# Performance work log

Measured on AMD Instinct MI355X. Metric: run time of the kernel, lower is better.

## Reference

```python
import jax, jax.numpy as jnp
import numpy as np

NUM_HEADS = 8
KEY_DIM = 32
ATTN_RATIO = 4
RESOLUTION = 7
VAL_DIM = KEY_DIM * ATTN_RATIO  # 128
SCALE = KEY_DIM ** (-0.5)


def _bias_idxs():
    # (2, N) grid positions, N = resolution^2
    r = RESOLUTION
    gh, gw = np.meshgrid(np.arange(r), np.arange(r), indexing='ij')
    pos = np.stack([gh, gw], 0).reshape(2, -1)
    rel = np.abs(pos[:, :, None] - pos[:, None, :])
    return jnp.asarray(rel[0] * r + rel[1], dtype=jnp.int32)  # (N, N)


def setup_inputs() -> dict:
    key = jax.random.key(0)
    ks = jax.random.split(key, 4)
    B, N, D = 2048, RESOLUTION * RESOLUTION, 384
    qkv_out = KEY_DIM * NUM_HEADS * 2 + VAL_DIM * NUM_HEADS  # 1536
    return {
        'x': jax.random.normal(ks[0], (B, N, D), jnp.float32),
        'qkv_kernel': jax.random.normal(ks[1], (D, qkv_out), jnp.float32) * 0.02,
        'qkv_bias': jnp.zeros((qkv_out,), jnp.float32),
        'proj_kernel': jax.random.normal(ks[2], (VAL_DIM * NUM_HEADS, D), jnp.float32) * 0.02,
        'proj_bias': jnp.zeros((D,), jnp.float32),
        'attention_biases': jax.random.normal(ks[3], (NUM_HEADS, N), jnp.float32) * 0.02,
    }


def reference(x, qkv_kernel, qkv_bias, proj_kernel, proj_bias, attention_biases):
    B, N, _ = x.shape
    idxs = _bias_idxs()  # (N, N) int32
    qkv = jnp.matmul(x, qkv_kernel) + qkv_bias            # (B, N, 1536)
    qkv = qkv.reshape(B, N, NUM_HEADS, -1).transpose(0, 2, 1, 3)  # (B, H, N, 2k+v)
    q = qkv[..., :KEY_DIM]
    k = qkv[..., KEY_DIM:2 * KEY_DIM]
    v = qkv[..., 2 * KEY_DIM:]
    attn = jnp.einsum('bhnd,bhmd->bhnm', q, k) * SCALE    # (B, H, N, N)
    bias = attention_biases[:, idxs]                       # (H, N, N) gather
    attn = jax.nn.softmax(attn + bias, axis=-1)
    out = jnp.einsum('bhnm,bhmd->bhnd', attn, v)           # (B, H, N, val_dim)
    out = out.transpose(0, 2, 1, 3).reshape(B, N, NUM_HEADS * VAL_DIM)
    return jnp.matmul(out, proj_kernel) + proj_bias
```

## Files before the change

kernel.cpp:

```cpp
#include <hip/hip_runtime.h>
#include <hip/hip_bf16.h>

using bf16x8 = short __attribute__((ext_vector_type(8)));
using f32x16 = float __attribute__((ext_vector_type(16)));

#define MROWS 100352
#define SCALE_Q 0.17677669529663687f
#define XCAST_BLOCKS 18816

static __device__ __forceinline__ unsigned short f2bs(float f){
  unsigned u = __builtin_bit_cast(unsigned, f);
  unsigned r = (u + 0x7FFFu + ((u >> 16) & 1u)) >> 16;
  return (unsigned short)r;
}
static __device__ __forceinline__ unsigned packbf(float a, float b){
  return (unsigned)f2bs(a) | ((unsigned)f2bs(b) << 16);
}

__global__ void k_prep(const float* __restrict__ x, const float* __restrict__ qkvW,
                       const float* __restrict__ qkvB, const float* __restrict__ projW,
                       const float* __restrict__ ab,
                       short* __restrict__ xb, short* __restrict__ WqkvT, short* __restrict__ WpT,
                       float* __restrict__ bqkv, float* __restrict__ bias_expT){
  const int bi = blockIdx.x;
  if (bi < XCAST_BLOCKS){
    const int i = bi*256 + threadIdx.x;
    const float4 u0 = *reinterpret_cast<const float4*>(x + (size_t)i*8);
    const float4 u1 = *reinterpret_cast<const float4*>(x + (size_t)i*8 + 4);
    bf16x8 t;
    t[0]=(short)f2bs(u0.x); t[1]=(short)f2bs(u0.y); t[2]=(short)f2bs(u0.z); t[3]=(short)f2bs(u0.w);
    t[4]=(short)f2bs(u1.x); t[5]=(short)f2bs(u1.y); t[6]=(short)f2bs(u1.z); t[7]=(short)f2bs(u1.w);
    *reinterpret_cast<bf16x8*>(xb + (size_t)i*8) = t;
    return;
  }
  int i = (bi - XCAST_BLOCKS)*256 + threadIdx.x;
  if (i < 1536*384){
    int c = i/384, f = i - c*384;
    int src; float sc = 1.0f;
    if (c < 512){ src = (c>>6)*192 + (c&63); if ((c&63) < 32) sc = SCALE_Q; }
    else        { int dv = c - 512; src = (dv>>7)*192 + 64 + (dv&127); }
    WqkvT[i] = (short)f2bs(qkvW[f*1536 + src] * sc);
    return;
  }
  i -= 1536*384;
  if (i < 384*1024){
    int j = i/1024, m = i - j*1024;
    WpT[i] = (short)f2bs(projW[m*384 + j]);
    return;
  }
  i -= 384*1024;
  if (i < 1536){
    int c = i; int src; float sc = 1.0f;
    if (c < 512){ src = (c>>6)*192 + (c&63); if ((c&63) < 32) sc = SCALE_Q; }
    else        { int dv = c - 512; src = (dv>>7)*192 + 64 + (dv&127); }
    bqkv[c] = qkvB[src] * sc;
    return;
  }
  i -= 1536;
  if (i < 8*49*64){
    int h = i / (49*64), rem = i - h*(49*64);
    int n = rem >> 6, r = rem & 63;
    float v = 0.0f;
    if (r < 49){
      int rh = r/7, rw = r - rh*7, ch = n/7, cw = n - ch*7;
      int dh = rh>ch?rh-ch:ch-rh, dw = rw>cw?rw-cw:cw-rw;
      v = ab[h*49 + dh*7 + dw];
    }
    bias_expT[i] = v;
  }
}

template<int KTOT, int NT, int NSLAB, bool F32OUT>
__global__ __launch_bounds__(512) void k_gemm(const short* __restrict__ A,
                                              const short* __restrict__ Bw,
                                              const float* __restrict__ bias,
                                              void* __restrict__ Cout, int ldc){
  constexpr int BN = NT*128;
  __shared__ short Alds[128*64];
  __shared__ short Blds[BN*64];
  const int lane = threadIdx.x & 63, w = threadIdx.x >> 6;
  const int hi = lane >> 5, l31 = lane & 31;
  const int wm = w >> 2, wn = w & 3;

  const int nwg = NSLAB * 784;
  const int lin = blockIdx.x + NSLAB * blockIdx.y;
  const int swz = (lin & 7) * (nwg >> 3) + (lin >> 3);
  const int slab = swz % NSLAB, panel = swz / NSLAB;
  const size_t R0 = (size_t)panel * 128, C0 = (size_t)slab * BN;

  f32x16 acc[2][NT];
  #pragma unroll
  for (int mt=0; mt<2; ++mt)
    #pragma unroll
    for (int nt=0; nt<NT; ++nt) acc[mt][nt] = (f32x16)0.0f;

  const int srow = lane >> 3;
  const int sG   = ((lane & 7) ^ srow) * 8;
  const short* aG = A  + (R0 + (size_t)(w*8 + srow))*KTOT + sG;
  const short* bG = Bw + (C0 + (size_t)(w*8 + srow))*KTOT + sG;

  constexpr int NK = KTOT/64;
  for (int kt=0; kt<NK; ++kt){
    #pragma unroll
    for (int j=0; j<2; ++j)
      __builtin_amdgcn_global_load_lds(
        (const unsigned int __attribute__((address_space(1)))*)(aG + (size_t)j*64*KTOT + kt*64),
        (unsigned int __attribute__((address_space(3)))*)(&Alds[(j*64 + w*8)*64]), 16, 0, 0);
    #pragma unroll
    for (int j=0; j<2*NT; ++j)
      __builtin_amdgcn_global_load_lds(
        (const unsigned int __attribute__((address_space(1)))*)(bG + (size_t)j*64*KTOT + kt*64),
        (unsigned int __attribute__((address_space(3)))*)(&Blds[(j*64 + w*8)*64]), 16, 0, 0);
    __syncthreads();
    #pragma unroll
    for (int ks=0; ks<4; ++ks){
      bf16x8 aF[2], bF[NT];
      #pragma unroll
      for (int mt=0; mt<2; ++mt){
        const int rA = wm*64 + mt*32 + l31;
        aF[mt] = *reinterpret_cast<const bf16x8*>(
                   (const char*)Alds + rA*128 + ((((ks<<1)|hi) ^ (rA&7))<<4));
      }
      #pragma unroll
      for (int nt=0; nt<NT; ++nt){
        const int rB = wn*(NT*32) + nt*32 + l31;
        bF[nt] = *reinterpret_cast<const bf16x8*>(
                   (const char*)Blds + rB*128 + ((((ks<<1)|hi) ^ (rB&7))<<4));
      }
      #pragma unroll
      for (int mt=0; mt<2; ++mt)
        #pragma unroll
        for (int nt=0; nt<NT; ++nt)
          acc[mt][nt] = __builtin_amdgcn_mfma_f32_32x32x16_bf16(aF[mt], bF[nt], acc[mt][nt], 0,0,0);
    }
    __syncthreads();
  }

  #pragma unroll
  for (int nt=0; nt<NT; ++nt){
    const int c = (int)C0 + wn*(NT*32) + nt*32 + l31;
    const float bb = bias[c];
    #pragma unroll
    for (int mt=0; mt<2; ++mt){
      const size_t rbase = R0 + wm*64 + mt*32;
      #pragma unroll
      for (int rg=0; rg<16; ++rg){
        const size_t r = rbase + (rg&3) + 8*(rg>>2) + 4*hi;
        if constexpr (F32OUT) ((float*)Cout)[r*ldc + c] = acc[mt][nt][rg] + bb;
        else                  ((short*)Cout)[r*ldc + c] = (short)f2bs(acc[mt][nt][rg] + bb);
      }
    }
  }
}

__global__ __launch_bounds__(256) void k_proj4(const short* __restrict__ A,
                                               const short* __restrict__ Bw,
                                               const float* __restrict__ bias,
                                               float* __restrict__ out){
  __shared__ short Alds[128*64];
  __shared__ short Blds[128*64];
  const int lane = threadIdx.x & 63, w = threadIdx.x >> 6;
  const int hi = lane >> 5, l31 = lane & 31;
  const int wm = w >> 1, wn = w & 1;

  const int nwg = 3 * 784;
  const int lin = blockIdx.x + 3 * blockIdx.y;
  const int swz = (lin & 7) * (nwg >> 3) + (lin >> 3);
  const int slab = swz % 3, panel = swz / 3;
  const size_t R0 = (size_t)panel * 128, C0 = (size_t)slab * 128;

  f32x16 acc[2][2];
  acc[0][0]=(f32x16)0.f; acc[0][1]=(f32x16)0.f; acc[1][0]=(f32x16)0.f; acc[1][1]=(f32x16)0.f;

  const int srow = lane >> 3;
  const int sG   = ((lane & 7) ^ srow) * 8;
  const short* aG = A  + (R0 + (size_t)(w*8 + srow))*1024 + sG;
  const short* bG = Bw + (C0 + (size_t)(w*8 + srow))*1024 + sG;

  for (int kt=0; kt<16; ++kt){
    #pragma unroll
    for (int j=0; j<4; ++j){
      __builtin_amdgcn_global_load_lds(
        (const unsigned int __attribute__((address_space(1)))*)(aG + (size_t)j*32*1024 + kt*64),
        (unsigned int __attribute__((address_space(3)))*)(&Alds[(j*32 + w*8)*64]), 16, 0, 0);
      __builtin_amdgcn_global_load_lds(
        (const unsigned int __attribute__((address_space(1)))*)(bG + (size_t)j*32*1024 + kt*64),
        (unsigned int __attribute__((address_space(3)))*)(&Blds[(j*32 + w*8)*64]), 16, 0, 0);
    }
    __syncthreads();
    #pragma unroll
    for (int ks=0; ks<4; ++ks){
      bf16x8 aF[2], bF[2];
      #pragma unroll
      for (int mt=0; mt<2; ++mt){
        const int rA = wm*64 + mt*32 + l31;
        aF[mt] = *reinterpret_cast<const bf16x8*>(
                   (const char*)Alds + rA*128 + ((((ks<<1)|hi) ^ (rA&7))<<4));
      }
      #pragma unroll
      for (int nt=0; nt<2; ++nt){
        const int rB = wn*64 + nt*32 + l31;
        bF[nt] = *reinterpret_cast<const bf16x8*>(
                   (const char*)Blds + rB*128 + ((((ks<<1)|hi) ^ (rB&7))<<4));
      }
      #pragma unroll
      for (int mt=0; mt<2; ++mt)
        #pragma unroll
        for (int nt=0; nt<2; ++nt)
          acc[mt][nt] = __builtin_amdgcn_mfma_f32_32x32x16_bf16(aF[mt], bF[nt], acc[mt][nt], 0,0,0);
    }
    __syncthreads();
  }

  #pragma unroll
  for (int nt=0; nt<2; ++nt){
    const int c = (int)C0 + wn*64 + nt*32 + l31;
    const float bb = bias[c];
    #pragma unroll
    for (int mt=0; mt<2; ++mt){
      const size_t rbase = R0 + wm*64 + mt*32;
      #pragma unroll
      for (int rg=0; rg<16; ++rg){
        const size_t r = rbase + (rg&3) + 8*(rg>>2) + 4*hi;
        out[r*384 + c] = acc[mt][nt][rg] + bb;
      }
    }
  }
}

__global__ __launch_bounds__(256) void k_attn(const short* __restrict__ qkvbuf,
                                              const float* __restrict__ bias_expT, short* __restrict__ aout){
  const int lane = threadIdx.x & 63, w = threadIdx.x >> 6;
  const int hi = lane >> 5, l31 = lane & 31;
  const int b = blockIdx.x, hg = blockIdx.y;
  const int h = hg*4 + w;

  __shared__ short vlds[4*49*136];

  for (int i=0; i<13; ++i){
    const int n = i*4 + w;
    if (n < 49){
      const bf16x8 vv = *reinterpret_cast<const bf16x8*>(qkvbuf + (b*49+n)*1536 + 512 + hg*512 + lane*8);
      const int hh = lane >> 4;
      const int d0 = ((lane & 15) * 8) ^ (((n>>3)&1) << 5);
      *reinterpret_cast<bf16x8*>(&vlds[(hh*49 + n)*136 + d0]) = vv;
    }
  }
  __syncthreads();

  bf16x8 kf[2][2];
  #pragma unroll
  for (int mt=0; mt<2; ++mt){
    const int n = 32*mt + l31;
    #pragma unroll
    for (int ks=0; ks<2; ++ks)
      kf[mt][ks] = (n < 49)
        ? *reinterpret_cast<const bf16x8*>(qkvbuf + (b*49+n)*1536 + h*64 + 32 + ks*16 + hi*8)
        : (bf16x8)(short)0;
  }
  const short* vb = &vlds[w*49*136];
  const int dxbase = hi << 5;

  for (int rb=0; rb<2; ++rb){
    const int r = 32*rb + l31;
    bf16x8 qf[2];
    #pragma unroll
    for (int ks=0; ks<2; ++ks)
      qf[ks] = (r < 49)
        ? *reinterpret_cast<const bf16x8*>(qkvbuf + (b*49+r)*1536 + h*64 + ks*16 + hi*8)
        : (bf16x8)(short)0;

    f32x16 s[2];
    s[0] = (f32x16)0.0f; s[1] = (f32x16)0.0f;
    #pragma unroll
    for (int ks=0; ks<2; ++ks){
      s[0] = __builtin_amdgcn_mfma_f32_32x32x16_bf16(kf[0][ks], qf[ks], s[0], 0, 0, 0);
      s[1] = __builtin_amdgcn_mfma_f32_32x32x16_bf16(kf[1][ks], qf[ks], s[1], 0, 0, 0);
    }

    float mloc = -3.0e38f;
    #pragma unroll
    for (int mt=0; mt<2; ++mt)
      #pragma unroll
      for (int rg=0; rg<16; ++rg){
        const int n = 32*mt + (rg&3) + 8*(rg>>2) + 4*hi;
        float v = s[mt][rg];
        v = (n < 49) ? v + bias_expT[(h*49 + n)*64 + r] : -1.0e30f;
        s[mt][rg] = v;
        mloc = fmaxf(mloc, v);
      }
    const float mrow = fmaxf(mloc, __shfl_xor(mloc, 32));
    float sloc = 0.0f;
    #pragma unroll
    for (int mt=0; mt<2; ++mt)
      #pragma unroll
      for (int rg=0; rg<16; ++rg){
        const float p = __expf(s[mt][rg] - mrow);
        s[mt][rg] = p; sloc += p;
      }
    const float inv = 1.0f / (sloc + __shfl_xor(sloc, 32));
    #pragma unroll
    for (int mt=0; mt<2; ++mt)
      #pragma unroll
      for (int rg=0; rg<16; ++rg) s[mt][rg] *= inv;

    unsigned pk[8][2];
    #pragma unroll
    for (int o=0; o<8; ++o){
      const int mt = o>>2, base = 4*(o&3);
      pk[o][0] = packbf(s[mt][base+0], s[mt][base+1]);
      pk[o][1] = packbf(s[mt][base+2], s[mt][base+3]);
    }
    bf16x8 af[4];
    #pragma unroll
    for (int ks=0; ks<4; ++ks){
      const unsigned e0 = pk[2*ks][0],   e1 = pk[2*ks][1];
      const unsigned o0 = pk[2*ks+1][0], o1 = pk[2*ks+1][1];
      const unsigned own0 = hi ? o0 : e0, own1 = hi ? o1 : e1;
      const unsigned oth0 = hi ? e0 : o0, oth1 = hi ? e1 : o1;
      const unsigned sw0 = __shfl_xor(oth0, 32), sw1 = __shfl_xor(oth1, 32);
      const unsigned lo0 = hi ? sw0 : own0, lo1 = hi ? sw1 : own1;
      const unsigned h0  = hi ? own0 : sw0, h1  = hi ? own1 : sw1;
      union { bf16x8 v; unsigned u[4]; } t;
      t.u[0]=lo0; t.u[1]=lo1; t.u[2]=h0; t.u[3]=h1;
      af[ks] = t.v;
    }

    #pragma unroll
    for (int dt=0; dt<4; ++dt){
      const int dx = (dt*32 + l31) ^ dxbase;
      f32x16 acc = (f32x16)0.0f;
      #pragma unroll
      for (int ks=0; ks<4; ++ks){
        bf16x8 t;
        if (ks < 3){
          const int nb = ks*16 + hi*8;
          #pragma unroll
          for (int j=0; j<8; ++j) t[j] = vb[(nb + j)*136 + dx];
        } else {
          #pragma unroll
          for (int j=0; j<8; ++j) t[j] = 0;
          if (hi == 0) t[0] = vb[48*136 + (dt*32 + l31)];
        }
        acc = __builtin_amdgcn_mfma_f32_32x32x16_bf16(af[ks], t, acc, 0, 0, 0);
      }
      #pragma unroll
      for (int rg=0; rg<16; ++rg){
        const int rr = 32*rb + (rg&3) + 8*(rg>>2) + 4*hi;
        if (rr < 49)
          aout[(b*49+rr)*1024 + h*128 + dt*32 + l31] = (short)f2bs(acc[rg]);
      }
    }
  }
}

extern "C" void kernel_launch(void* const* d_in, const int* in_sizes, int n_in,
                              void* d_out, int out_size, void* d_ws, size_t ws_size,
                              hipStream_t stream) {
  const float* x     = (const float*)d_in[0];
  const float* qkvW  = (const float*)d_in[1];
  const float* qkvB  = (const float*)d_in[2];
  const float* projW = (const float*)d_in[3];
  const float* projB = (const float*)d_in[4];
  const float* ab    = (const float*)d_in[5];

  char* ws = (char*)d_ws;
  short* aoutb = (short*)ws;
  short* xb    = (short*)ws;
  size_t off = (size_t)MROWS*1024*2;
  short* qkvbuf = (short*)(ws + off); off += (size_t)MROWS*1536*2;
  short* WqkvT  = (short*)(ws + off); off += (size_t)1536*384*2;
  short* WpT    = (short*)(ws + off); off += (size_t)384*1024*2;
  float* bqkv   = (float*)(ws + off); off += (size_t)1536*4;
  float* bias_expT = (float*)(ws + off); off += (size_t)8*49*64*4;
  if (ws_size < off) return;

  const int conv_total = 1536*384 + 384*1024 + 1536 + 8*49*64;
  const int prep_blocks = XCAST_BLOCKS + (conv_total + 255)/256;
  k_prep<<<prep_blocks, 256, 0, stream>>>(x, qkvW, qkvB, projW, ab,
                                          xb, WqkvT, WpT, bqkv, bias_expT);
  k_gemm<384, 2, 6, false><<<dim3(6, 784), 512, 0, stream>>>(xb, WqkvT, bqkv, qkvbuf, 1536);
  k_attn<<<dim3(2048, 2), 256, 0, stream>>>(qkvbuf, bias_expT, aoutb);
  k_proj4<<<dim3(3, 784), 256, 0, stream>>>(aoutb, WpT, projB, (float*)d_out);
}
```

Baseline: 505.0 us.

## Rewrite QKV GEMM with 256x256 tiles and triple-buffered LDS pipeline

Replaces the generic QKV GEMM with a dedicated kernel that uses 256x256 output tiles, K-steps of 32, and three LDS buffers. Global-to-LDS loads for step kt+2 are issued between the two MFMA halves, with vmcnt waits and a single barrier per step so data movement overlaps compute. MFMA sections also raise wave priority. The larger tile raises reuse, but 96KB of LDS per block and more accumulators per wave limit occupancy.

Measured after the change: 504.4 us. Within noise of the previous version (-0.1%).

```diff
diff --git a/kernel.cpp b/kernel.cpp
--- a/kernel.cpp
+++ b/kernel.cpp
@@ -70,84 +70,116 @@
   }
 }
 
-template<int KTOT, int NT, int NSLAB, bool F32OUT>
-__global__ __launch_bounds__(512) void k_gemm(const short* __restrict__ A,
-                                              const short* __restrict__ Bw,
-                                              const float* __restrict__ bias,
-                                              void* __restrict__ Cout, int ldc){
-  constexpr int BN = NT*128;
-  __shared__ short Alds[128*64];
-  __shared__ short Blds[BN*64];
-  const int lane = threadIdx.x & 63, w = threadIdx.x >> 6;
+__global__ __launch_bounds__(512) void k_qkv7(const short* __restrict__ xb,
+                                              const short* __restrict__ WqkvT,
+                                              const float* __restrict__ bqkv,
+                                              short* __restrict__ qkvbuf){
+  __shared__ short lds3[3][512*32];
+  const int t = threadIdx.x;
+  const int lane = t & 63, w = t >> 6;
   const int hi = lane >> 5, l31 = lane & 31;
-  const int wm = w >> 2, wn = w & 3;
-
-  const int nwg = NSLAB * 784;
-  const int lin = blockIdx.x + NSLAB * blockIdx.y;
-  const int swz = (lin & 7) * (nwg >> 3) + (lin >> 3);
-  const int slab = swz % NSLAB, panel = swz / NSLAB;
-  const size_t R0 = (size_t)panel * 128, C0 = (size_t)slab * BN;
-
-  f32x16 acc[2][NT];
+  const int wm = w >> 1, wn = w & 1;
+
+  const int nwg = 6*392;
+  const int lin = blockIdx.x + 6*blockIdx.y;
+  const int swz = (lin & 7)*(nwg>>3) + (lin>>3);
+  const int slab = swz % 6, panel = swz / 6;
+  const size_t R0 = (size_t)panel*256, C0 = (size_t)slab*256;
+
+  const int srowl  = lane >> 2;
+  const int schunk = ((lane & 3) ^ ((lane >> 3) & 3)) * 8;
+  const short* aG0 = xb    + (R0 + (size_t)(w*16       + srowl))*384 + schunk;
+  const short* aG1 = xb    + (R0 + (size_t)((8+w)*16   + srowl))*384 + schunk;
+  const short* bG0 = WqkvT + (C0 + (size_t)(w*16       + srowl))*384 + schunk;
+  const short* bG1 = WqkvT + (C0 + (size_t)((8+w)*16   + srowl))*384 + schunk;
+
+  auto stage = [&](int bufi, int kti){
+    short* base = &lds3[bufi][0];
+    __builtin_amdgcn_global_load_lds((const unsigned __attribute__((address_space(1)))*)(aG0 + kti*32),
+        (unsigned __attribute__((address_space(3)))*)(base + w*512), 16, 0, 0);
+    __builtin_amdgcn_global_load_lds((const unsigned __attribute__((address_space(1)))*)(aG1 + kti*32),
+        (unsigned __attribute__((address_space(3)))*)(base + (8+w)*512), 16, 0, 0);
+    __builtin_amdgcn_global_load_lds((const unsigned __attribute__((address_space(1)))*)(bG0 + kti*32),
+        (unsigned __attribute__((address_space(3)))*)(base + 8192 + w*512), 16, 0, 0);
+    __builtin_amdgcn_global_load_lds((const unsigned __attribute__((address_space(1)))*)(bG1 + kti*32),
+        (unsigned __attribute__((address_space(3)))*)(base + 8192 + (8+w)*512), 16, 0, 0);
+  };
+
+  f32x16 acc[2][4];
   #pragma unroll
   for (int mt=0; mt<2; ++mt)
     #pragma unroll
-    for (int nt=0; nt<NT; ++nt) acc[mt][nt] = (f32x16)0.0f;
-
-  const int srow = lane >> 3;
-  const int sG   = ((lane & 7) ^ srow) * 8;
-  const short* aG = A  + (R0 + (size_t)(w*8 + srow))*KTOT + sG;
-  const short* bG = Bw + (C0 + (size_t)(w*8 + srow))*KTOT + sG;
-
-  constexpr int NK = KTOT/64;
-  for (int kt=0; kt<NK; ++kt){
-    #pragma unroll
-    for (int j=0; j<2; ++j)
-      __builtin_amdgcn_global_load_lds(
-        (const unsigned int __attribute__((address_space(1)))*)(aG + (size_t)j*64*KTOT + kt*64),
-        (unsigned int __attribute__((address_space(3)))*)(&Alds[(j*64 + w*8)*64]), 16, 0, 0);
-    #pragma unroll
-    for (int j=0; j<2*NT; ++j)
-      __builtin_amdgcn_global_load_lds(
-        (const unsigned int __attribute__((address_space(1)))*)(bG + (size_t)j*64*KTOT + kt*64),
-        (unsigned int __attribute__((address_space(3)))*)(&Blds[(j*64 + w*8)*64]), 16, 0, 0);
-    __syncthreads();
-    #pragma unroll
-    for (int ks=0; ks<4; ++ks){
-      bf16x8 aF[2], bF[NT];
+    for (int nt=0; nt<4; ++nt) acc[mt][nt] = (f32x16)0.0f;
+
+  stage(0, 0); stage(1, 1);
+
+  int cur = 0;
+  for (int kt=0; kt<12; ++kt){
+    if (kt < 11) asm volatile("s_waitcnt vmcnt(4)" ::: "memory");
+    else         asm volatile("s_waitcnt vmcnt(0)" ::: "memory");
+    __builtin_amdgcn_s_barrier();
+
+    const char* Ab = (const char*)&lds3[cur][0];
+    const char* Bb = Ab + 16384;
+
+    {
+      bf16x8 aF[2], bF[4];
       #pragma unroll
       for (int mt=0; mt<2; ++mt){
         const int rA = wm*64 + mt*32 + l31;
-        aF[mt] = *reinterpret_cast<const bf16x8*>(
-                   (const char*)Alds + rA*128 + ((((ks<<1)|hi) ^ (rA&7))<<4));
-      }
-      #pragma unroll
-      for (int nt=0; nt<NT; ++nt){
-        const int rB = wn*(NT*32) + nt*32 + l31;
-        bF[nt] = *reinterpret_cast<const bf16x8*>(
-                   (const char*)Blds + rB*128 + ((((ks<<1)|hi) ^ (rB&7))<<4));
-      }
+        aF[mt] = *reinterpret_cast<const bf16x8*>(Ab + rA*64 + (((0|hi) ^ ((rA>>1)&3))<<4));
+      }
+      #pragma unroll
+      for (int nt=0; nt<4; ++nt){
+        const int rB = wn*128 + nt*32 + l31;
+        bF[nt] = *reinterpret_cast<const bf16x8*>(Bb + rB*64 + (((0|hi) ^ ((rB>>1)&3))<<4));
+      }
+      __builtin_amdgcn_s_setprio(1);
       #pragma unroll
       for (int mt=0; mt<2; ++mt)
         #pragma unroll
-        for (int nt=0; nt<NT; ++nt)
+        for (int nt=0; nt<4; ++nt)
           acc[mt][nt] = __builtin_amdgcn_mfma_f32_32x32x16_bf16(aF[mt], bF[nt], acc[mt][nt], 0,0,0);
-    }
-    __syncthreads();
+      __builtin_amdgcn_s_setprio(0);
+    }
+    if (kt < 10){
+      const int nb = (cur + 2 >= 3) ? cur - 1 : cur + 2;
+      stage(nb, kt + 2);
+    }
+    {
+      bf16x8 aF[2], bF[4];
+      #pragma unroll
+      for (int mt=0; mt<2; ++mt){
+        const int rA = wm*64 + mt*32 + l31;
+        aF[mt] = *reinterpret_cast<const bf16x8*>(Ab + rA*64 + (((2|hi) ^ ((rA>>1)&3))<<4));
+      }
+      #pragma unroll
+      for (int nt=0; nt<4; ++nt){
+        const int rB = wn*128 + nt*32 + l31;
+        bF[nt] = *reinterpret_cast<const bf16x8*>(Bb + rB*64 + (((2|hi) ^ ((rB>>1)&3))<<4));
+      }
+      __builtin_amdgcn_s_setprio(1);
+      #pragma unroll
+      for (int mt=0; mt<2; ++mt)
+        #pragma unroll
+        for (int nt=0; nt<4; ++nt)
+          acc[mt][nt] = __builtin_amdgcn_mfma_f32_32x32x16_bf16(aF[mt], bF[nt], acc[mt][nt], 0,0,0);
+      __builtin_amdgcn_s_setprio(0);
+    }
+    cur = (cur == 2) ? 0 : cur + 1;
   }
 
   #pragma unroll
-  for (int nt=0; nt<NT; ++nt){
-    const int c = (int)C0 + wn*(NT*32) + nt*32 + l31;
-    const float bb = bias[c];
+  for (int nt=0; nt<4; ++nt){
+    const int c = (int)C0 + wn*128 + nt*32 + l31;
+    const float bb = bqkv[c];
     #pragma unroll
     for (int mt=0; mt<2; ++mt){
       const size_t rbase = R0 + wm*64 + mt*32;
       #pragma unroll
       for (int rg=0; rg<16; ++rg){
         const size_t r = rbase + (rg&3) + 8*(rg>>2) + 4*hi;
-        if constexpr (F32OUT) ((float*)Cout)[r*ldc + c] = acc[mt][nt][rg] + bb;
-        else                  ((short*)Cout)[r*ldc + c] = (short)f2bs(acc[mt][nt][rg] + bb);
+        qkvbuf[r*1536 + c] = (short)f2bs(acc[mt][nt][rg] + bb);
       }
     }
   }
@@ -379,7 +411,7 @@
   const int prep_blocks = XCAST_BLOCKS + (conv_total + 255)/256;
   k_prep<<<prep_blocks, 256, 0, stream>>>(x, qkvW, qkvB, projW, ab,
                                           xb, WqkvT, WpT, bqkv, bias_expT);
-  k_gemm<384, 2, 6, false><<<dim3(6, 784), 512, 0, stream>>>(xb, WqkvT, bqkv, qkvbuf, 1536);
+  k_qkv7<<<dim3(6, 392), 512, 0, stream>>>(xb, WqkvT, bqkv, qkvbuf);
   k_attn<<<dim3(2048, 2), 256, 0, stream>>>(qkvbuf, bias_expT, aoutb);
   k_proj4<<<dim3(3, 784), 256, 0, stream>>>(aoutb, WpT, projB, (float*)d_out);
 }
```
